# Kernel tuning notes

Measured on AMD Instinct MI355X. Metric: run time of the kernel, lower is better.

The kernel has to match this reference:

```python
import jax, jax.numpy as jnp
import numpy as np


def setup_inputs() -> dict:
    key = jax.random.key(0)
    k1, k2, k3 = jax.random.split(key, 3)
    Q, N, D = 2048, 100000, 512
    x = jax.random.normal(k1, (Q, D), dtype=jnp.float32)
    target_embeddings = jax.random.normal(k2, (N, D), dtype=jnp.float32)
    target_labels = jax.random.randint(k3, (N,), 0, 400, dtype=jnp.int64)
    return {"x": x, "target_embeddings": target_embeddings,
            "target_labels": target_labels, "k": 5}


def reference(x, target_embeddings, target_labels, k):
    # torch.cdist(x[:,None], T[None], p=2).squeeze(1): full [Q, N] euclidean distances
    x2 = jnp.sum(x * x, axis=-1, keepdims=True)            # [Q, 1]
    t2 = jnp.sum(target_embeddings * target_embeddings, axis=-1)  # [N]
    d2 = x2 + t2[None, :] - 2.0 * (x @ target_embeddings.T)       # [Q, N]
    dist = jnp.sqrt(jnp.maximum(d2, 0.0))
    # topk smallest distances
    neg_vals, topk_inds = jax.lax.top_k(-dist, k)           # [Q, k]
    topk_dists = -neg_vals
    # pred = target_labels[inds].t() in the original eval path
    pred = target_labels[topk_inds].T                       # [k, Q]
    return topk_dists, topk_inds, pred
```

## Files before the change

kernel.cpp:

```cpp
#include <hip/hip_runtime.h>
#include <float.h>
#include <math.h>

#define NQ 2048
#define NT 100000
#define DIM 512
#define KTOP 5
#define NCAND 16
#define QTILE 128
#define TTILE 128
#define NTPC 13
#define NCH 64
#define TBLKS 782
#define QBLKS 16
#define NSUB 6
#define CV_TBLKS (TBLKS*16)
#define CV_XBLKS ((NQ/128)*16)

typedef float f32x4 __attribute__((ext_vector_type(4)));
typedef short s16x8 __attribute__((ext_vector_type(8)));
typedef unsigned int u32;
typedef unsigned short u16;

__device__ __forceinline__ int tsub_start(int ts) { return (13 * ts + 5) / 6; }

__device__ __forceinline__ bool lt_pair(float v1, int i1, float v2, int i2) {
  return v1 < v2 || (v1 == v2 && i1 < i2);
}

__device__ __forceinline__ void ins5(float* tv, int* tix, float sc, int idx) {
  if (lt_pair(sc, idx, tv[4], tix[4])) {
    tv[4] = sc; tix[4] = idx;
#pragma unroll
    for (int p = 4; p > 0; --p)
      if (lt_pair(tv[p], tix[p], tv[p - 1], tix[p - 1])) {
        float tf = tv[p]; tv[p] = tv[p - 1]; tv[p - 1] = tf;
        int tn = tix[p]; tix[p] = tix[p - 1]; tix[p - 1] = tn;
      }
  }
}

__device__ __forceinline__ void merge5(float* av, int* ai, const float* bv, const int* bi) {
  float nv[5]; int ni[5];
#pragma unroll
  for (int s = 0; s < 5; ++s) {
    if (lt_pair(av[s], ai[s], bv[4 - s], bi[4 - s])) { nv[s] = av[s]; ni[s] = ai[s]; }
    else { nv[s] = bv[4 - s]; ni[s] = bi[4 - s]; }
  }
#pragma unroll
  for (int a = 0; a < 5; ++a)
#pragma unroll
    for (int b = 0; b < 4 - a; ++b)
      if (lt_pair(nv[b + 1], ni[b + 1], nv[b], ni[b])) {
        float tf = nv[b]; nv[b] = nv[b + 1]; nv[b + 1] = tf;
        int tn = ni[b]; ni[b] = ni[b + 1]; ni[b + 1] = tn;
      }
#pragma unroll
  for (int s = 0; s < 5; ++s) { av[s] = nv[s]; ai[s] = ni[s]; }
}

__global__ __launch_bounds__(256) void convert_kernel(
    const float* __restrict__ x, const float* __restrict__ T,
    short* __restrict__ xhi, short* __restrict__ thi,
    float* __restrict__ t2, float* __restrict__ x2) {
  __shared__ short lh[4096];
  const int bid = blockIdx.x;
  const bool isT = bid < CV_TBLKS;
  const int task = isT ? bid : bid - CV_TBLKS;
  const int blk = task >> 4, kbi = task & 15;
  const float* src = isT ? T : x;
  short* dhi = isT ? thi : xhi;
  float* nrm = isT ? t2 : x2;
  const int nsrc = isT ? NT : NQ;

  const int t = threadIdx.x;
  const int rr = t >> 1, half = t & 1;
  const int grow = blk * 128 + rr;
  const int rs = grow < nsrc ? grow : nsrc - 1;
  const float* p = src + (size_t)rs * DIM + kbi * 32 + half * 16;
  f32x4 v[4];
#pragma unroll
  for (int i = 0; i < 4; ++i) v[i] = ((const f32x4*)p)[i];

  float ss = 0.f;
#pragma unroll
  for (int g = 0; g < 2; ++g) {
    s16x8 hv;
#pragma unroll
    for (int e = 0; e < 8; ++e) {
      int i = g * 8 + e;
      float f = v[i >> 2][i & 3];
      ss = fmaf(f, f, ss);
      u32 u = __builtin_bit_cast(u32, f);
      u32 r1 = u + 0x7FFFu + ((u >> 16) & 1u);
      hv[e] = (short)(r1 >> 16);
    }
    int unit = (rr >> 4) * 64 + (half * 2 + g) * 16 + (rr & 15);
    *(s16x8*)(lh + unit * 8) = hv;
  }
  ss += __shfl_xor(ss, 1, 64);
  if (half == 0 && grow < nsrc) atomicAdd(nrm + grow, ss);

  __syncthreads();
  size_t obase = ((size_t)(blk * 16 + kbi)) * 4096 + t * 16;
  *(s16x8*)(dhi + obase)     = *(const s16x8*)(lh + t * 16);
  *(s16x8*)(dhi + obase + 8) = *(const s16x8*)(lh + t * 16 + 8);
}

__global__ __launch_bounds__(256, 3) void knn_mfma(
    const short* __restrict__ xhi, const short* __restrict__ thi,
    const float* __restrict__ t2g,
    float* __restrict__ pvals, u16* __restrict__ pidx16) {
  __shared__ float scr_all[4 * 1280];

  const int tid = threadIdx.x;
  const int w = tid >> 6;
  const int l = tid & 63;
  const int bid = blockIdx.x;
  const u32 rest = (u32)bid >> 3;
  const int inner = (int)(rest % 96u);
  const int chunk = (bid & 7) + 8 * (int)(rest / 96u);
  const int qblk = inner & 15;
  const int tsub = inner >> 4;
  const int tstart = tsub_start(tsub);
  const int tend = tsub_start(tsub + 1);
  const int q0 = qblk * QTILE;
  const int wr = (w >> 1) * 64;
  const int wc = (w & 1) * 64;
  const int arow = wr >> 4;
  const int bcol = wc >> 4;

  const s16x8* xh8 = (const s16x8*)xhi;
  const s16x8* th8 = (const s16x8*)thi;

  float tv[KTOP]; int tix[KTOP];
#pragma unroll
  for (int s = 0; s < KTOP; ++s) { tv[s] = FLT_MAX; tix[s] = 0x7FFFFFFF; }

#pragma unroll 1
  for (int tt = tstart; tt < tend; ++tt) {
    const int bblk = chunk * NTPC + tt;
    if (bblk >= TBLKS) continue;
    const int jbase = bblk * TTILE;
    f32x4 acc[4][4];
#pragma unroll
    for (int i = 0; i < 4; ++i)
#pragma unroll
      for (int j = 0; j < 4; ++j) acc[i][j] = (f32x4){0.f, 0.f, 0.f, 0.f};

    u32 offA = (u32)(qblk * 16) * 512u + (u32)(arow * 64 + l);
    u32 offB = (u32)(bblk * 16) * 512u + (u32)(bcol * 64 + l);
    s16x8 ah[4], bh[4];
#pragma unroll 1
    for (int kbi = 0; kbi < 16; ++kbi) {
#pragma unroll
      for (int i = 0; i < 4; ++i) {
        ah[i] = xh8[offA + i * 64];
        bh[i] = th8[offB + i * 64];
      }
      offA += 512; offB += 512;
      __builtin_amdgcn_s_setprio(1);
#pragma unroll
      for (int j = 0; j < 4; ++j)
#pragma unroll
        for (int i = 0; i < 4; ++i)
          acc[i][j] = __builtin_amdgcn_mfma_f32_16x16x32_bf16(ah[i], bh[j], acc[i][j], 0, 0, 0);
      __builtin_amdgcn_s_setprio(0);
    }

    float* scr = scr_all + w * 1280;
#pragma unroll
    for (int jj = 0; jj < 4; ++jj) {
      int colg = jbase + wc + jj * 16 + (l & 15);
      int cc = colg < NT ? colg : NT - 1;
      float t2v = t2g[cc];
      bool valid = colg < NT;
#pragma unroll
      for (int i = 0; i < 4; ++i)
#pragma unroll
        for (int r = 0; r < 4; ++r) {
          float sc = valid ? fmaf(-2.f, acc[i][jj][r], t2v) : FLT_MAX;
          int rowl = i * 16 + ((l >> 4) << 2) + r;
          scr[rowl * 20 + (l & 15)] = sc;
        }
      int cbg = jbase + wc + jj * 16;
#pragma unroll
      for (int c4 = 0; c4 < 4; ++c4) {
        f32x4 rv = *(const f32x4*)(scr + l * 20 + c4 * 4);
#pragma unroll
        for (int c = 0; c < 4; ++c) ins5(tv, tix, rv[c], cbg + c4 * 4 + c);
      }
    }
  }

  __syncthreads();
  float* ms = scr_all;
  int* msi = (int*)scr_all + 640;
  if (w & 1) {
    int rid = wr + l;
#pragma unroll
    for (int s = 0; s < KTOP; ++s) { ms[rid * 5 + s] = tv[s]; msi[rid * 5 + s] = tix[s]; }
  }
  __syncthreads();
  if (!(w & 1)) {
    int rid = wr + l;
    float ov[KTOP]; int oi[KTOP];
#pragma unroll
    for (int s = 0; s < KTOP; ++s) { ov[s] = ms[rid * 5 + s]; oi[s] = msi[rid * 5 + s]; }
    merge5(tv, tix, ov, oi);
    int q = q0 + rid;
    const int blockBase = (chunk * NTPC + tstart) * TTILE;
    size_t base = ((size_t)q * (NCH * NSUB) + (chunk * NSUB + tsub)) * KTOP;
#pragma unroll
    for (int s = 0; s < KTOP; ++s) {
      pvals[base + s] = tv[s];
      pidx16[base + s] = (u16)(tix[s] - blockBase);
    }
  }
}

__global__ __launch_bounds__(256) void knn_merge16(
    const float* __restrict__ pvals, const u16* __restrict__ pidx16,
    int* __restrict__ idx16g) {
  const int M = NCH * NSUB * KTOP;
  int q = (blockIdx.x * 256 + threadIdx.x) >> 6;
  int l = threadIdx.x & 63;
  if (q >= NQ) return;
  float v[30]; int ix[30];
  size_t base = (size_t)q * M;
#pragma unroll
  for (int j = 0; j < 30; ++j) {
    int m = j * 64 + l;
    int slot = m / KTOP;
    int ch = slot / NSUB, ts = slot % NSUB;
    int gb = (ch * NTPC + tsub_start(ts)) * TTILE;
    v[j] = pvals[base + m];
    ix[j] = gb + (int)pidx16[base + m];
  }
  int mywin = 0x7FFFFFFF;
#pragma unroll 1
  for (int r = 0; r < NCAND; ++r) {
    float bv = FLT_MAX; int bi = 0x7FFFFFFF;
#pragma unroll
    for (int j = 0; j < 30; ++j)
      if (lt_pair(v[j], ix[j], bv, bi)) { bv = v[j]; bi = ix[j]; }
#pragma unroll
    for (int d = 1; d < 64; d <<= 1) {
      float ov = __shfl_xor(bv, d, 64);
      int oi = __shfl_xor(bi, d, 64);
      if (lt_pair(ov, oi, bv, bi)) { bv = ov; bi = oi; }
    }
    if (l == r) mywin = bi;
#pragma unroll
    for (int j = 0; j < 30; ++j)
      if (ix[j] == bi) v[j] = FLT_MAX;
  }
  if (l < NCAND) idx16g[q * NCAND + l] = mywin;
}

__global__ __launch_bounds__(256) void knn_rerank(
    const float* __restrict__ x, const float* __restrict__ T,
    const int* __restrict__ idx16g, const int* __restrict__ labels,
    float* __restrict__ out) {
  __shared__ float sd2[4 * NCAND];
  __shared__ int sti[4 * NCAND];
  const int w = threadIdx.x >> 6, l = threadIdx.x & 63;
  const int q = blockIdx.x * 4 + w;
  const int cand = l >> 2, sub = l & 3;
  const int ti = idx16g[q * NCAND + cand];
  const f32x4* tp = (const f32x4*)(T + (size_t)ti * DIM + sub * 128);
  const f32x4* xp = (const f32x4*)(x + (size_t)q * DIM + sub * 128);
  float dot = 0.f, tt = 0.f, xx = 0.f;
#pragma unroll
  for (int i = 0; i < 32; ++i) {
    f32x4 a = xp[i], b = tp[i];
#pragma unroll
    for (int c = 0; c < 4; ++c) {
      dot = fmaf(a[c], b[c], dot);
      tt  = fmaf(b[c], b[c], tt);
      xx  = fmaf(a[c], a[c], xx);
    }
  }
#pragma unroll
  for (int d = 1; d < 4; d <<= 1) {
    dot += __shfl_xor(dot, d, 64);
    tt  += __shfl_xor(tt, d, 64);
    xx  += __shfl_xor(xx, d, 64);
  }
  if (sub == 0) { sd2[w * NCAND + cand] = xx + tt - 2.f * dot; sti[w * NCAND + cand] = ti; }
  __syncthreads();
  if (l == 0) {
    float tv[KTOP]; int tix[KTOP];
#pragma unroll
    for (int s = 0; s < KTOP; ++s) { tv[s] = FLT_MAX; tix[s] = 0x7FFFFFFF; }
#pragma unroll
    for (int c = 0; c < NCAND; ++c) ins5(tv, tix, sd2[w * NCAND + c], sti[w * NCAND + c]);
#pragma unroll
    for (int s = 0; s < KTOP; ++s) {
      float d2 = tv[s] > 0.f ? tv[s] : 0.f;
      out[(size_t)q * KTOP + s] = sqrtf(d2);
      out[(size_t)NQ * KTOP + (size_t)q * KTOP + s] = (float)tix[s];
      out[(size_t)2 * NQ * KTOP + (size_t)s * NQ + q] =
          (float)labels[tix[s]];
    }
  }
}

extern "C" void kernel_launch(void* const* d_in, const int* in_sizes, int n_in,
                              void* d_out, int out_size, void* d_ws, size_t ws_size,
                              hipStream_t stream) {
  const float* x = (const float*)d_in[0];
  const float* T = (const float*)d_in[1];
  const int* labels = (const int*)d_in[2];
  float* out = (float*)d_out;
  char* ws = (char*)d_ws;

  float* t2    = (float*)(ws + 0);
  float* x2    = (float*)(ws + 401408);
  short* xhi   = (short*)(ws + 409600);
  short* thi   = (short*)(ws + 2506752);
  float* pvals = (float*)(ws + 105005056);
  u16*   pidx16 = (u16*)(ws + 120733696);
  int*   idx16g = (int*)(ws + 128598016);

  hipMemsetAsync(ws, 0, 409600, stream);

  convert_kernel<<<CV_TBLKS + CV_XBLKS, 256, 0, stream>>>(
      x, T, xhi, thi, t2, x2);

  knn_mfma<<<QBLKS * NSUB * NCH, 256, 0, stream>>>(
      xhi, thi, t2, pvals, pidx16);

  knn_merge16<<<(NQ * 64 + 255) / 256, 256, 0, stream>>>(pvals, pidx16, idx16g);

  knn_rerank<<<NQ / 4, 256, 0, stream>>>(x, T, idx16g, labels, out);
}
```

Measured before the change: 684.7 us.

## Swap MFMA operand roles to keep per-lane top-5 in registers, halve sub-splits

Targets now serve as MFMA A operand and queries as B, so each lane's accumulator rows map to targets for fixed query columns. This lets each lane keep four register top-5 lists fed directly from accumulators, replacing the LDS scratch transpose, followed by cross-lane shuffle merges and one LDS merge across waves. The target range per block is doubled (NSUB 6→3), which halves the number of partial results and the merge kernel's work. The cost is more register pressure (occupancy hint lowered from 3 to 2) and fewer blocks launched.

```diff
diff --git a/kernel.cpp b/kernel.cpp
--- a/kernel.cpp
+++ b/kernel.cpp
@@ -13,7 +13,7 @@
 #define NCH 64
 #define TBLKS 782
 #define QBLKS 16
-#define NSUB 6
+#define NSUB 3
 #define CV_TBLKS (TBLKS*16)
 #define CV_XBLKS ((NQ/128)*16)
 
@@ -22,10 +22,22 @@
 typedef unsigned int u32;
 typedef unsigned short u16;
 
-__device__ __forceinline__ int tsub_start(int ts) { return (13 * ts + 5) / 6; }
+__device__ __forceinline__ int tsub_start(int ts) { return (13 * ts + 2) / 3; }
 
 __device__ __forceinline__ bool lt_pair(float v1, int i1, float v2, int i2) {
   return v1 < v2 || (v1 == v2 && i1 < i2);
+}
+
+__device__ __forceinline__ void ins5f(float* tv, int* tix, float sc, int idx) {
+  if (sc < tv[4]) {
+    tv[4] = sc; tix[4] = idx;
+#pragma unroll
+    for (int p = 4; p > 0; --p)
+      if (tv[p] < tv[p - 1]) {
+        float tf = tv[p]; tv[p] = tv[p - 1]; tv[p - 1] = tf;
+        int tn = tix[p]; tix[p] = tix[p - 1]; tix[p - 1] = tn;
+      }
+  }
 }
 
 __device__ __forceinline__ void ins5(float* tv, int* tix, float sc, int idx) {
@@ -107,19 +119,20 @@
   *(s16x8*)(dhi + obase + 8) = *(const s16x8*)(lh + t * 16 + 8);
 }
 
-__global__ __launch_bounds__(256, 3) void knn_mfma(
+__global__ __launch_bounds__(256, 2) void knn_mfma(
     const short* __restrict__ xhi, const short* __restrict__ thi,
     const float* __restrict__ t2g,
     float* __restrict__ pvals, u16* __restrict__ pidx16) {
-  __shared__ float scr_all[4 * 1280];
+  __shared__ float msv[128 * 5];
+  __shared__ int   msi[128 * 5];
 
   const int tid = threadIdx.x;
   const int w = tid >> 6;
   const int l = tid & 63;
   const int bid = blockIdx.x;
   const u32 rest = (u32)bid >> 3;
-  const int inner = (int)(rest % 96u);
-  const int chunk = (bid & 7) + 8 * (int)(rest / 96u);
+  const int inner = (int)(rest % 48u);
+  const int chunk = (bid & 7) + 8 * (int)(rest / 48u);
   const int qblk = inner & 15;
   const int tsub = inner >> 4;
   const int tstart = tsub_start(tsub);
@@ -133,30 +146,32 @@
   const s16x8* xh8 = (const s16x8*)xhi;
   const s16x8* th8 = (const s16x8*)thi;
 
-  float tv[KTOP]; int tix[KTOP];
-#pragma unroll
-  for (int s = 0; s < KTOP; ++s) { tv[s] = FLT_MAX; tix[s] = 0x7FFFFFFF; }
+  float tv4[4][KTOP]; int tix4[4][KTOP];
+#pragma unroll
+  for (int jj = 0; jj < 4; ++jj)
+#pragma unroll
+    for (int s = 0; s < KTOP; ++s) { tv4[jj][s] = FLT_MAX; tix4[jj][s] = 0x7FFFFFFF; }
 
 #pragma unroll 1
   for (int tt = tstart; tt < tend; ++tt) {
     const int bblk = chunk * NTPC + tt;
     if (bblk >= TBLKS) continue;
-    const int jbase = bblk * TTILE;
+    const int tbase = bblk * TTILE;
     f32x4 acc[4][4];
 #pragma unroll
     for (int i = 0; i < 4; ++i)
 #pragma unroll
       for (int j = 0; j < 4; ++j) acc[i][j] = (f32x4){0.f, 0.f, 0.f, 0.f};
 
-    u32 offA = (u32)(qblk * 16) * 512u + (u32)(arow * 64 + l);
-    u32 offB = (u32)(bblk * 16) * 512u + (u32)(bcol * 64 + l);
+    u32 offA = (u32)(bblk * 16) * 512u + (u32)(arow * 64 + l);
+    u32 offB = (u32)(qblk * 16) * 512u + (u32)(bcol * 64 + l);
     s16x8 ah[4], bh[4];
 #pragma unroll 1
     for (int kbi = 0; kbi < 16; ++kbi) {
 #pragma unroll
       for (int i = 0; i < 4; ++i) {
-        ah[i] = xh8[offA + i * 64];
-        bh[i] = th8[offB + i * 64];
+        ah[i] = th8[offA + i * 64];
+        bh[i] = xh8[offB + i * 64];
       }
       offA += 512; offB += 512;
       __builtin_amdgcn_s_setprio(1);
@@ -168,53 +183,68 @@
       __builtin_amdgcn_s_setprio(0);
     }
 
-    float* scr = scr_all + w * 1280;
+    const int tg0 = tbase + wr + ((l >> 4) << 2);
+    float t2v[16];
+#pragma unroll
+    for (int i = 0; i < 4; ++i)
+#pragma unroll
+      for (int r = 0; r < 4; ++r) {
+        int t = tg0 + i * 16 + r;
+        float vv = t2g[t < NT ? t : NT - 1];
+        t2v[i * 4 + r] = t < NT ? vv : FLT_MAX;
+      }
+#pragma unroll
+    for (int jj = 0; jj < 4; ++jj)
+#pragma unroll
+      for (int i = 0; i < 4; ++i)
+#pragma unroll
+        for (int r = 0; r < 4; ++r) {
+          float sc = fmaf(-2.f, acc[i][jj][r], t2v[i * 4 + r]);
+          ins5f(tv4[jj], tix4[jj], sc, tg0 + i * 16 + r);
+        }
+  }
+
+#pragma unroll
+  for (int jj = 0; jj < 4; ++jj)
+#pragma unroll
+    for (int d = 16; d <= 32; d <<= 1) {
+      float ov[KTOP]; int oi[KTOP];
+#pragma unroll
+      for (int s = 0; s < KTOP; ++s) {
+        ov[s] = __shfl_xor(tv4[jj][s], d, 64);
+        oi[s] = __shfl_xor(tix4[jj][s], d, 64);
+      }
+      merge5(tv4[jj], tix4[jj], ov, oi);
+    }
+
+  const int blockBase = (chunk * NTPC + tstart) * TTILE;
+  if ((w >> 1) && (l >> 4) == 0) {
 #pragma unroll
     for (int jj = 0; jj < 4; ++jj) {
-      int colg = jbase + wc + jj * 16 + (l & 15);
-      int cc = colg < NT ? colg : NT - 1;
-      float t2v = t2g[cc];
-      bool valid = colg < NT;
-#pragma unroll
-      for (int i = 0; i < 4; ++i)
-#pragma unroll
-        for (int r = 0; r < 4; ++r) {
-          float sc = valid ? fmaf(-2.f, acc[i][jj][r], t2v) : FLT_MAX;
-          int rowl = i * 16 + ((l >> 4) << 2) + r;
-          scr[rowl * 20 + (l & 15)] = sc;
-        }
-      int cbg = jbase + wc + jj * 16;
-#pragma unroll
-      for (int c4 = 0; c4 < 4; ++c4) {
-        f32x4 rv = *(const f32x4*)(scr + l * 20 + c4 * 4);
-#pragma unroll
-        for (int c = 0; c < 4; ++c) ins5(tv, tix, rv[c], cbg + c4 * 4 + c);
-      }
-    }
-  }
-
+      int qr = wc + jj * 16 + l;
+#pragma unroll
+      for (int s = 0; s < KTOP; ++s) {
+        msv[qr * 5 + s] = tv4[jj][s];
+        msi[qr * 5 + s] = tix4[jj][s];
+      }
+    }
+  }
   __syncthreads();
-  float* ms = scr_all;
-  int* msi = (int*)scr_all + 640;
-  if (w & 1) {
-    int rid = wr + l;
-#pragma unroll
-    for (int s = 0; s < KTOP; ++s) { ms[rid * 5 + s] = tv[s]; msi[rid * 5 + s] = tix[s]; }
-  }
-  __syncthreads();
-  if (!(w & 1)) {
-    int rid = wr + l;
-    float ov[KTOP]; int oi[KTOP];
-#pragma unroll
-    for (int s = 0; s < KTOP; ++s) { ov[s] = ms[rid * 5 + s]; oi[s] = msi[rid * 5 + s]; }
-    merge5(tv, tix, ov, oi);
-    int q = q0 + rid;
-    const int blockBase = (chunk * NTPC + tstart) * TTILE;
-    size_t base = ((size_t)q * (NCH * NSUB) + (chunk * NSUB + tsub)) * KTOP;
-#pragma unroll
-    for (int s = 0; s < KTOP; ++s) {
-      pvals[base + s] = tv[s];
-      pidx16[base + s] = (u16)(tix[s] - blockBase);
+  if (!(w >> 1) && (l >> 4) == 0) {
+#pragma unroll
+    for (int jj = 0; jj < 4; ++jj) {
+      int qr = wc + jj * 16 + l;
+      float ov[KTOP]; int oi[KTOP];
+#pragma unroll
+      for (int s = 0; s < KTOP; ++s) { ov[s] = msv[qr * 5 + s]; oi[s] = msi[qr * 5 + s]; }
+      merge5(tv4[jj], tix4[jj], ov, oi);
+      int q = q0 + qr;
+      size_t base = ((size_t)q * (NCH * NSUB) + (chunk * NSUB + tsub)) * KTOP;
+#pragma unroll
+      for (int s = 0; s < KTOP; ++s) {
+        pvals[base + s] = tv4[jj][s];
+        pidx16[base + s] = (u16)(tix4[jj][s] - blockBase);
+      }
     }
   }
 }
@@ -226,10 +256,10 @@
   int q = (blockIdx.x * 256 + threadIdx.x) >> 6;
   int l = threadIdx.x & 63;
   if (q >= NQ) return;
-  float v[30]; int ix[30];
+  float v[15]; int ix[15];
   size_t base = (size_t)q * M;
 #pragma unroll
-  for (int j = 0; j < 30; ++j) {
+  for (int j = 0; j < 15; ++j) {
     int m = j * 64 + l;
     int slot = m / KTOP;
     int ch = slot / NSUB, ts = slot % NSUB;
@@ -242,7 +272,7 @@
   for (int r = 0; r < NCAND; ++r) {
     float bv = FLT_MAX; int bi = 0x7FFFFFFF;
 #pragma unroll
-    for (int j = 0; j < 30; ++j)
+    for (int j = 0; j < 15; ++j)
       if (lt_pair(v[j], ix[j], bv, bi)) { bv = v[j]; bi = ix[j]; }
 #pragma unroll
     for (int d = 1; d < 64; d <<= 1) {
@@ -252,7 +282,7 @@
     }
     if (l == r) mywin = bi;
 #pragma unroll
-    for (int j = 0; j < 30; ++j)
+    for (int j = 0; j < 15; ++j)
       if (ix[j] == bi) v[j] = FLT_MAX;
   }
   if (l < NCAND) idx16g[q * NCAND + l] = mywin;
@@ -315,13 +345,13 @@
   float* out = (float*)d_out;
   char* ws = (char*)d_ws;
 
-  float* t2    = (float*)(ws + 0);
-  float* x2    = (float*)(ws + 401408);
-  short* xhi   = (short*)(ws + 409600);
-  short* thi   = (short*)(ws + 2506752);
-  float* pvals = (float*)(ws + 105005056);
-  u16*   pidx16 = (u16*)(ws + 120733696);
-  int*   idx16g = (int*)(ws + 128598016);
+  float* t2     = (float*)(ws + 0);
+  float* x2     = (float*)(ws + 401408);
+  short* xhi    = (short*)(ws + 409600);
+  short* thi    = (short*)(ws + 2506752);
+  float* pvals  = (float*)(ws + 105005056);
+  u16*   pidx16 = (u16*)(ws + 112869376);
+  int*   idx16g = (int*)(ws + 116801536);
 
   hipMemsetAsync(ws, 0, 409600, stream);
 
```

After: 693.1 us. About the same (+1.2%).
